# Kernel tuning notes

Hardware: AMD Instinct MI355X
Metric: run time of the kernel (lower is better)

## Reference

```python
import jax, jax.numpy as jnp
import numpy as np

EPS = 1e-12  # tf.math.l2_normalize epsilon


def get_posenc(n, d):
    # Standard sinusoidal positional encoding, shape [n, d].
    pos = np.arange(n)[:, None].astype(np.float32)
    i = np.arange(d)[None, :]
    angle_rates = 1.0 / np.power(10000.0, (2 * (i // 2)).astype(np.float32) / np.float32(d))
    angles = pos * angle_rates
    pe = np.zeros((n, d), dtype=np.float32)
    pe[:, 0::2] = np.sin(angles[:, 0::2])
    pe[:, 1::2] = np.cos(angles[:, 1::2])
    return jnp.asarray(pe)


def setup_inputs() -> dict:
    key = jax.random.key(0)
    k1, k2, k3 = jax.random.split(key, 3)
    B, N, D = 4, 2048, 2048  # N must equal D (model_size) for the posenc matmul
    data = jax.random.normal(k1, (B, N, D), dtype=jnp.float32)
    W_exp = jax.random.normal(k2, (D + 1, D), dtype=jnp.float32) * (1.0 / np.sqrt(D + 1))
    b_exp = jnp.zeros((D,), dtype=jnp.float32)
    W_merge = jax.random.normal(k3, (2 * D, D), dtype=jnp.float32) * (1.0 / np.sqrt(2 * D))
    return {"data": data, "W_exp": W_exp, "b_exp": b_exp, "W_merge": W_merge}


def reference(data, W_exp, b_exp, W_merge):
    B, N, D = data.shape
    # l2 normalize along feature dim
    sq = jnp.sum(data * data, axis=-1, keepdims=True)
    cn = data * jax.lax.rsqrt(jnp.maximum(sq, EPS))
    # pairwise cosine similarity, rectified: [B, N, N]
    sim = jax.nn.relu(jnp.einsum("bnd,bmd->bnm", cn, cn))
    # fixed positional matmul: posenc [N, D] with D == N -> [B, N, N]
    fixed_v = get_posenc(N, D)
    v_output = jnp.einsum("nk,bkm->bnm", fixed_v, sim)
    # row-sum of similarities: [B, N, 1]
    csum = jnp.sum(sim, axis=-1, keepdims=True)
    counter = jnp.concatenate([csum, v_output], axis=-1)  # [B, N, N+1]
    counter = jax.nn.softplus(counter @ W_exp + b_exp)  # [B, N, D]
    out = jnp.concatenate([data, counter], axis=-1) @ W_merge  # [B, N, D]
    return out
```

## Files before the change

### kernel.cpp

```cpp
#include <hip/hip_runtime.h>

#define B_ 4
#define N_ 2048
#define D_ 2048

#define BM 128
#define BN 128
#define BK 32
#define TP 136

typedef __bf16 bf16x8 __attribute__((ext_vector_type(8)));
typedef float  f32x4  __attribute__((ext_vector_type(4)));

__device__ __forceinline__ ushort f2bf(float x) {
  union { float f; unsigned u; } c; c.f = x;
  unsigned u = c.u;
  u += 0x7fffu + ((u >> 16) & 1u);
  return (ushort)(u >> 16);
}

__device__ __forceinline__ void gld16(ushort* lds, const ushort* g) {
  __builtin_amdgcn_global_load_lds(
      (const __attribute__((address_space(1))) void*)g,
      (__attribute__((address_space(3))) void*)lds, 16, 0, 0);
}


__global__ void prep_cn(const float* __restrict__ data, ushort* __restrict__ cn,
                        ushort* __restrict__ catA) {
  const int row = blockIdx.x;
  const long base = (long)row * D_;
  const float4* r4 = (const float4*)(data + base);
  const int tid = threadIdx.x;
  float4 u0 = r4[tid * 2], u1 = r4[tid * 2 + 1];
  float s = u0.x*u0.x + u0.y*u0.y + u0.z*u0.z + u0.w*u0.w
          + u1.x*u1.x + u1.y*u1.y + u1.z*u1.z + u1.w*u1.w;
  #pragma unroll
  for (int o = 32; o > 0; o >>= 1) s += __shfl_down(s, o);
  __shared__ float wsum[4];
  if ((tid & 63) == 0) wsum[tid >> 6] = s;
  __syncthreads();
  const float tot = wsum[0] + wsum[1] + wsum[2] + wsum[3];
  const float sc = rsqrtf(fmaxf(tot, 1e-12f));
  uint4 pc, pd;
  pc.x = (unsigned)f2bf(u0.x * sc) | ((unsigned)f2bf(u0.y * sc) << 16);
  pc.y = (unsigned)f2bf(u0.z * sc) | ((unsigned)f2bf(u0.w * sc) << 16);
  pc.z = (unsigned)f2bf(u1.x * sc) | ((unsigned)f2bf(u1.y * sc) << 16);
  pc.w = (unsigned)f2bf(u1.z * sc) | ((unsigned)f2bf(u1.w * sc) << 16);
  pd.x = (unsigned)f2bf(u0.x) | ((unsigned)f2bf(u0.y) << 16);
  pd.y = (unsigned)f2bf(u0.z) | ((unsigned)f2bf(u0.w) << 16);
  pd.z = (unsigned)f2bf(u1.x) | ((unsigned)f2bf(u1.y) << 16);
  pd.w = (unsigned)f2bf(u1.z) | ((unsigned)f2bf(u1.w) << 16);
  *(uint4*)(cn + base + tid * 8) = pc;
  *(uint4*)(catA + (long)row * (2 * D_) + tid * 8) = pd;
}

__global__ void prep_pe(ushort* __restrict__ pe) {
  const int id = blockIdx.x * 256 + threadIdx.x;
  const int n = id >> 11, d = id & (D_ - 1);
  const float e = (float)(2 * (d >> 1)) * (1.0f / (float)D_);
  const float rate = expf(e * -9.210340371976184f);
  const float ang = (float)n * rate;
  const float v = (d & 1) ? cosf(ang) : sinf(ang);
  pe[id] = f2bf(v);
}

__global__ void transpose_bf16(const float* __restrict__ in, ushort* __restrict__ out,
                               int R, int C) {
  __shared__ float t[32][33];
  const int c0 = blockIdx.x * 32, r0 = blockIdx.y * 32;
  const int tx = threadIdx.x, ty = threadIdx.y;
  #pragma unroll
  for (int i = 0; i < 32; i += 8) t[ty + i][tx] = in[(long)(r0 + ty + i) * C + c0 + tx];
  __syncthreads();
  #pragma unroll
  for (int i = 0; i < 32; i += 8) out[(long)(c0 + ty + i) * R + r0 + tx] = f2bf(t[tx][ty + i]);
}

__global__ __launch_bounds__(256, 2) void gemm_sym(
    const ushort* __restrict__ Ag, ushort* __restrict__ Cg, float* __restrict__ csum) {
  __shared__ ushort sAt[BM * BK];
  __shared__ ushort sBt[BN * BK];
  __shared__ ushort tile[128 * TP];

  const int bz = blockIdx.z;
  const int t = blockIdx.x;
  int bj = (int)((sqrtf(8.f * (float)t + 1.f) - 1.f) * 0.5f);
  while ((bj + 1) * (bj + 2) / 2 <= t) bj++;
  while (bj * (bj + 1) / 2 > t) bj--;
  const int bi = t - bj * (bj + 1) / 2;

  const ushort* A = Ag + (long)bz * N_ * D_;
  const int blockRow = bi * BM;
  const int blockCol = bj * BN;

  const int tid = threadIdx.x;
  const int w = tid >> 6, L = tid & 63;
  const int ldRow = w * 16 + (L >> 2);
  const int ldK = (((L & 3) ^ ((L >> 3) & 3)) * 8);
  const ushort* a0 = A + (long)(blockRow + ldRow) * D_ + ldK;
  const ushort* a1 = a0 + (long)64 * D_;
  const ushort* b0 = A + (long)(blockCol + ldRow) * D_ + ldK;
  const ushort* b1 = b0 + (long)64 * D_;
  ushort* sA0 = sAt + w * 512;
  ushort* sA1 = sAt + 2048 + w * 512;
  ushort* sB0 = sBt + w * 512;
  ushort* sB1 = sBt + 2048 + w * 512;

  const int wm = (w & 1) * 64, wn = (w >> 1) * 64;
  const int fr = L & 15;
  const int sw = (((L >> 4) ^ ((fr >> 1) & 3)) * 8);

  f32x4 acc[4][4] = {};
  for (int k0 = 0; k0 < D_; k0 += BK) {
    gld16(sA0, a0); gld16(sA1, a1);
    gld16(sB0, b0); gld16(sB1, b1);
    a0 += BK; a1 += BK; b0 += BK; b1 += BK;
    __syncthreads();
    bf16x8 af[4], bfv[4];
    #pragma unroll
    for (int i = 0; i < 4; i++) af[i]  = *(const bf16x8*)&sAt[(wm + i * 16 + fr) * BK + sw];
    #pragma unroll
    for (int j = 0; j < 4; j++) bfv[j] = *(const bf16x8*)&sBt[(wn + j * 16 + fr) * BK + sw];
    #pragma unroll
    for (int i = 0; i < 4; i++)
      #pragma unroll
      for (int j = 0; j < 4; j++)
        acc[i][j] = __builtin_amdgcn_mfma_f32_16x16x32_bf16(af[i], bfv[j], acc[i][j], 0, 0, 0);
    __syncthreads();
  }

  const int rq = (L >> 4) * 4;
  const int cq = L & 15;
  ushort* C = Cg + (long)bz * N_ * N_;

  float rs[4][4];
  float cs[4];
  #pragma unroll
  for (int i = 0; i < 4; i++)
    #pragma unroll
    for (int r = 0; r < 4; r++) rs[i][r] = 0.f;
  #pragma unroll
  for (int j = 0; j < 4; j++) cs[j] = 0.f;

  const bool offdiag = (bi != bj);
  #pragma unroll
  for (int i = 0; i < 4; i++)
    #pragma unroll
    for (int j = 0; j < 4; j++)
      #pragma unroll
      for (int r = 0; r < 4; r++) {
        const float v = fmaxf(acc[i][j][r], 0.f);
        const int lrow = wm + i * 16 + rq + r;
        const int lcol = wn + j * 16 + cq;
        const ushort bv = f2bf(v);
        C[(long)(blockRow + lrow) * N_ + blockCol + lcol] = bv;
        rs[i][r] += v;
        cs[j] += v;
        if (offdiag) tile[lcol * TP + lrow] = bv;
      }

  #pragma unroll
  for (int i = 0; i < 4; i++)
    #pragma unroll
    for (int r = 0; r < 4; r++) {
      float s = rs[i][r];
      s += __shfl_xor(s, 1); s += __shfl_xor(s, 2);
      s += __shfl_xor(s, 4); s += __shfl_xor(s, 8);
      if (cq == 0)
        atomicAdd(&csum[(long)bz * N_ + blockRow + wm + i * 16 + rq + r], s);
    }

  if (offdiag) {
    #pragma unroll
    for (int j = 0; j < 4; j++) {
      float s = cs[j];
      s += __shfl_xor(s, 16); s += __shfl_xor(s, 32);
      if (L < 16)
        atomicAdd(&csum[(long)bz * N_ + blockCol + wn + j * 16 + cq], s);
    }
    __syncthreads();
    const int rp = tid >> 1, h = tid & 1;
    const ushort* src = &tile[rp * TP + h * 64];
    ushort* dst = &C[(long)(blockCol + rp) * N_ + blockRow + h * 64];
    #pragma unroll
    for (int q = 0; q < 8; q++)
      *(uint4*)(dst + q * 8) = *(const uint4*)(src + q * 8);
  }
}

template <int MODE>
__global__ __launch_bounds__(256, 2) void gemm_bt(
    const ushort* __restrict__ Ag, const ushort* __restrict__ Bg, void* __restrict__ Cg,
    int K, long sA, long sB, long sC, int ldc, int colOff,
    const float* __restrict__ csum, const float* __restrict__ w0,
    const float* __restrict__ bexp) {
  __shared__ ushort sAt[BM * BK];
  __shared__ ushort sBt[BN * BK];

  const int lin = blockIdx.x + (blockIdx.y << 4) + (blockIdx.z << 8);
  const int xcd = lin & 7, m = lin >> 3;
  const int bz = xcd >> 1;
  const int by = ((xcd & 1) << 3) + (m >> 4);
  const int bx = m & 15;

  const ushort* A  = Ag + (long)bz * sA;
  const ushort* Bp = Bg + (long)bz * sB;

  const int tid = threadIdx.x;
  const int w = tid >> 6, L = tid & 63;
  const int blockRow = bx * BM;
  const int blockCol = by * BN;

  const int ldRow = w * 16 + (L >> 2);
  const int ldK = (((L & 3) ^ ((L >> 3) & 3)) * 8);
  const ushort* a0 = A  + (long)(blockRow + ldRow) * K + ldK;
  const ushort* a1 = a0 + (long)64 * K;
  const ushort* b0 = Bp + (long)(blockCol + ldRow) * K + ldK;
  const ushort* b1 = b0 + (long)64 * K;
  ushort* sA0 = sAt + w * 512;
  ushort* sA1 = sAt + 2048 + w * 512;
  ushort* sB0 = sBt + w * 512;
  ushort* sB1 = sBt + 2048 + w * 512;

  const int wm = (w & 1) * 64, wn = (w >> 1) * 64;
  const int fr = L & 15;
  const int sw = (((L >> 4) ^ ((fr >> 1) & 3)) * 8);

  f32x4 acc[4][4] = {};
  for (int k0 = 0; k0 < K; k0 += BK) {
    gld16(sA0, a0); gld16(sA1, a1);
    gld16(sB0, b0); gld16(sB1, b1);
    a0 += BK; a1 += BK; b0 += BK; b1 += BK;
    __syncthreads();
    bf16x8 af[4], bfv[4];
    #pragma unroll
    for (int i = 0; i < 4; i++) af[i]  = *(const bf16x8*)&sAt[(wm + i * 16 + fr) * BK + sw];
    #pragma unroll
    for (int j = 0; j < 4; j++) bfv[j] = *(const bf16x8*)&sBt[(wn + j * 16 + fr) * BK + sw];
    #pragma unroll
    for (int i = 0; i < 4; i++)
      #pragma unroll
      for (int j = 0; j < 4; j++)
        acc[i][j] = __builtin_amdgcn_mfma_f32_16x16x32_bf16(af[i], bfv[j], acc[i][j], 0, 0, 0);
    __syncthreads();
  }

  const int rq = (L >> 4) * 4;
  const int cq = L & 15;

  if (MODE == 1) {
    ushort* C = (ushort*)Cg + (long)bz * sC;
    #pragma unroll
    for (int i = 0; i < 4; i++)
      #pragma unroll
      for (int j = 0; j < 4; j++)
        #pragma unroll
        for (int r = 0; r < 4; r++) {
          const int row = blockRow + wm + i * 16 + rq + r;
          const int col = blockCol + wn + j * 16 + cq;
          C[(long)row * ldc + col] = f2bf(acc[i][j][r]);
        }
  } else if (MODE == 2) {
    ushort* C = (ushort*)Cg + (long)bz * sC;
    #pragma unroll
    for (int i = 0; i < 4; i++)
      #pragma unroll
      for (int j = 0; j < 4; j++)
        #pragma unroll
        for (int r = 0; r < 4; r++) {
          const int row = blockRow + wm + i * 16 + rq + r;
          const int col = blockCol + wn + j * 16 + cq;
          const float x = acc[i][j][r] + csum[(long)bz * N_ + row] * w0[col] + bexp[col];
          const float sp = fmaxf(x, 0.f) + log1pf(expf(-fabsf(x)));
          C[(long)row * ldc + colOff + col] = f2bf(sp);
        }
  } else {
    float* C = (float*)Cg + (long)bz * sC;
    #pragma unroll
    for (int i = 0; i < 4; i++)
      #pragma unroll
      for (int j = 0; j < 4; j++)
        #pragma unroll
        for (int r = 0; r < 4; r++) {
          const int row = blockRow + wm + i * 16 + rq + r;
          const int col = blockCol + wn + j * 16 + cq;
          C[(long)row * ldc + col] = acc[i][j][r];
        }
  }
}

extern "C" void kernel_launch(void* const* d_in, const int* in_sizes, int n_in,
                              void* d_out, int out_size, void* d_ws, size_t ws_size,
                              hipStream_t stream) {
  const float* data    = (const float*)d_in[0];
  const float* W_exp   = (const float*)d_in[1];
  const float* b_exp   = (const float*)d_in[2];
  const float* W_merge = (const float*)d_in[3];

  char* ws = (char*)d_ws;
  const size_t MB = 1024 * 1024;
  ushort* cnv  = (ushort*)(ws);
  ushort* sim  = (ushort*)(ws + 32 * MB);
  ushort* pe   = (ushort*)(ws + 64 * MB);
  ushort* weT  = (ushort*)(ws + 72 * MB);
  ushort* wmT  = (ushort*)(ws + 80 * MB);
  ushort* catA = (ushort*)(ws + 96 * MB);
  float*  csum = (float*)(ws + 160 * MB);

  hipMemsetAsync(csum, 0, (size_t)B_ * N_ * sizeof(float), stream);
  prep_cn<<<B_ * N_, 256, 0, stream>>>(data, cnv, catA);
  prep_pe<<<(N_ * N_) / 256, 256, 0, stream>>>(pe);
  transpose_bf16<<<dim3(D_ / 32, D_ / 32), dim3(32, 8), 0, stream>>>(W_exp + D_, weT, D_, D_);
  transpose_bf16<<<dim3(D_ / 32, (2 * D_) / 32), dim3(32, 8), 0, stream>>>(W_merge, wmT, 2 * D_, D_);

  dim3 blk(256);
  gemm_sym<<<dim3(136, 1, B_), blk, 0, stream>>>(cnv, sim, csum);
  dim3 g(N_ / BM, N_ / BN, B_);
  gemm_bt<1><<<g, blk, 0, stream>>>(pe, sim, cnv, N_, 0, (long)N_ * N_,
                                    (long)N_ * N_, N_, 0, nullptr, nullptr, nullptr);
  gemm_bt<2><<<g, blk, 0, stream>>>(cnv, weT, catA, N_, (long)N_ * N_, 0,
                                    (long)N_ * 2 * D_, 2 * D_, D_, csum, W_exp, b_exp);
  gemm_bt<3><<<g, blk, 0, stream>>>(catA, wmT, d_out, 2 * D_, (long)N_ * 2 * D_, 0,
                                    (long)N_ * D_, D_, 0, nullptr, nullptr, nullptr);
}
```

Baseline: 561.9 us.

## Replace 128x128 GEMMs with 256x256 eight-wave double-buffered pipelined kernel

Replaces the three dense bf16 GEMMs with a 256x256-tile, 512-thread kernel. It uses 128KB of dynamic LDS with double-buffered BK=64 stages, and interleaves global-to-LDS prefetch with MFMA phases under explicit barriers, vmcnt waits and setprio. The aim is more data reuse per tile and hiding of load latency behind compute, where the old kernel waited on each K step with two syncthreads. In exchange, the larger tiles mean fewer blocks (256 per GEMM) and occupancy is limited by LDS. The hand-scheduled waitcnt logic is fragile.

```diff
diff --git a/kernel.cpp b/kernel.cpp
--- a/kernel.cpp
+++ b/kernel.cpp
@@ -189,103 +189,153 @@
   }
 }
 
+
+__device__ __forceinline__ void stage_half(ushort* d, const ushort* s, int K) {
+  gld16(d, s);
+  gld16(d + 4096, s + (long)64 * K);
+}
+
+template <int M0, bool FIRST, class STG>
+__device__ __forceinline__ void phase8(const ushort* __restrict__ TA,
+                                       const ushort* __restrict__ TB,
+                                       int aO0, int aO1, int bO0, int bO1,
+                                       bf16x8 (&bf)[4][2], f32x4 (&acc)[8][4],
+                                       int vm, STG&& stg) {
+  if (FIRST) {
+    #pragma unroll
+    for (int j = 0; j < 4; j++) {
+      bf[j][0] = *(const bf16x8*)&TB[bO0 + j * 1024];
+      bf[j][1] = *(const bf16x8*)&TB[bO1 + j * 1024];
+    }
+  }
+  bf16x8 af[2][2];
+  #pragma unroll
+  for (int mm = 0; mm < 2; mm++) {
+    af[mm][0] = *(const bf16x8*)&TA[aO0 + (M0 + mm) * 1024];
+    af[mm][1] = *(const bf16x8*)&TA[aO1 + (M0 + mm) * 1024];
+  }
+  __builtin_amdgcn_sched_barrier(0);
+  stg();
+  asm volatile("s_barrier" ::: "memory");
+  asm volatile("s_waitcnt lgkmcnt(0)" ::: "memory");
+  __builtin_amdgcn_sched_barrier(0);
+  __builtin_amdgcn_s_setprio(1);
+  #pragma unroll
+  for (int kk = 0; kk < 2; kk++)
+    #pragma unroll
+    for (int mm = 0; mm < 2; mm++)
+      #pragma unroll
+      for (int j = 0; j < 4; j++)
+        acc[M0 + mm][j] = __builtin_amdgcn_mfma_f32_16x16x32_bf16(
+            af[mm][kk], bf[j][kk], acc[M0 + mm][j], 0, 0, 0);
+  __builtin_amdgcn_s_setprio(0);
+  if (vm == 6)      asm volatile("s_waitcnt vmcnt(6)" ::: "memory");
+  else if (vm == 0) asm volatile("s_waitcnt vmcnt(0)" ::: "memory");
+  asm volatile("s_barrier" ::: "memory");
+}
+
 template <int MODE>
-__global__ __launch_bounds__(256, 2) void gemm_bt(
+__global__ __launch_bounds__(512, 2) void gemm8(
     const ushort* __restrict__ Ag, const ushort* __restrict__ Bg, void* __restrict__ Cg,
     int K, long sA, long sB, long sC, int ldc, int colOff,
     const float* __restrict__ csum, const float* __restrict__ w0,
     const float* __restrict__ bexp) {
-  __shared__ ushort sAt[BM * BK];
-  __shared__ ushort sBt[BN * BK];
-
-  const int lin = blockIdx.x + (blockIdx.y << 4) + (blockIdx.z << 8);
-  const int xcd = lin & 7, m = lin >> 3;
+  extern __shared__ ushort lds[];
+
+  const int lin = blockIdx.x + (blockIdx.y << 3) + (blockIdx.z << 6);
+  const int xcd = lin & 7, m_ = lin >> 3;
   const int bz = xcd >> 1;
-  const int by = ((xcd & 1) << 3) + (m >> 4);
-  const int bx = m & 15;
-
-  const ushort* A  = Ag + (long)bz * sA;
-  const ushort* Bp = Bg + (long)bz * sB;
+  const int by = ((xcd & 1) << 2) + (m_ >> 3);
+  const int bx = m_ & 7;
+
+  const ushort* A  = Ag + (long)bz * sA + (long)(bx << 8) * K;
+  const ushort* Bp = Bg + (long)bz * sB + (long)(by << 8) * K;
 
   const int tid = threadIdx.x;
-  const int w = tid >> 6, L = tid & 63;
-  const int blockRow = bx * BM;
-  const int blockCol = by * BN;
-
-  const int ldRow = w * 16 + (L >> 2);
-  const int ldK = (((L & 3) ^ ((L >> 3) & 3)) * 8);
-  const ushort* a0 = A  + (long)(blockRow + ldRow) * K + ldK;
-  const ushort* a1 = a0 + (long)64 * K;
-  const ushort* b0 = Bp + (long)(blockCol + ldRow) * K + ldK;
-  const ushort* b1 = b0 + (long)64 * K;
-  ushort* sA0 = sAt + w * 512;
-  ushort* sA1 = sAt + 2048 + w * 512;
-  ushort* sB0 = sBt + w * 512;
-  ushort* sB1 = sBt + 2048 + w * 512;
-
-  const int wm = (w & 1) * 64, wn = (w >> 1) * 64;
-  const int fr = L & 15;
-  const int sw = (((L >> 4) ^ ((fr >> 1) & 3)) * 8);
-
-  f32x4 acc[4][4] = {};
-  for (int k0 = 0; k0 < K; k0 += BK) {
-    gld16(sA0, a0); gld16(sA1, a1);
-    gld16(sB0, b0); gld16(sB1, b1);
-    a0 += BK; a1 += BK; b0 += BK; b1 += BK;
-    __syncthreads();
-    bf16x8 af[4], bfv[4];
-    #pragma unroll
-    for (int i = 0; i < 4; i++) af[i]  = *(const bf16x8*)&sAt[(wm + i * 16 + fr) * BK + sw];
-    #pragma unroll
-    for (int j = 0; j < 4; j++) bfv[j] = *(const bf16x8*)&sBt[(wn + j * 16 + fr) * BK + sw];
-    #pragma unroll
-    for (int i = 0; i < 4; i++)
-      #pragma unroll
-      for (int j = 0; j < 4; j++)
-        acc[i][j] = __builtin_amdgcn_mfma_f32_16x16x32_bf16(af[i], bfv[j], acc[i][j], 0, 0, 0);
-    __syncthreads();
-  }
-
-  const int rq = (L >> 4) * 4;
-  const int cq = L & 15;
-
-  if (MODE == 1) {
-    ushort* C = (ushort*)Cg + (long)bz * sC;
-    #pragma unroll
-    for (int i = 0; i < 4; i++)
+  const int sr = tid >> 3;
+  const int sc = ((tid & 7) ^ (sr & 7)) << 3;
+  const ushort* aS = A + (long)sr * K + sc;
+  const ushort* bS = Bp + (long)sr * K + sc;
+  const int wOff = (tid >> 6) << 9;
+  ushort* const stA0 = lds + wOff;
+  ushort* const stA1 = lds + 16384 + wOff;
+  ushort* const stB0 = lds + 32768 + wOff;
+  ushort* const stB1 = lds + 49152 + wOff;
+  const ushort* const TA0 = lds;          const ushort* const TA1 = lds + 16384;
+  const ushort* const TB0 = lds + 32768;  const ushort* const TB1 = lds + 49152;
+
+  auto stg = [&](ushort* base, const ushort* src, int T, int H) {
+    stage_half(base + (H << 13), src + (long)(H << 7) * K + ((long)T << 6), K);
+  };
+
+  const int L = tid & 63, wid = tid >> 6;
+  const int wr = wid >> 2, wc = wid & 3;
+  const int fr = L & 15, g = L >> 4;
+  const int off0 = ((g ^ (fr & 7)) << 3);
+  const int aO0 = ((wr << 7) + fr) * 64 + off0, aO1 = aO0 ^ 32;
+  const int bO0 = ((wc << 6) + fr) * 64 + off0, bO1 = bO0 ^ 32;
+
+  f32x4 acc[8][4] = {};
+  bf16x8 bf[4][2];
+
+  const int NT = K >> 6, NTI = NT >> 1;
+
+  stg(stB0, bS, 0, 0); stg(stB0, bS, 0, 1); stg(stA0, aS, 0, 0); stg(stA0, aS, 0, 1);
+  stg(stB1, bS, 1, 0); stg(stB1, bS, 1, 1); stg(stA1, aS, 1, 0); stg(stA1, aS, 1, 1);
+  asm volatile("s_waitcnt vmcnt(6)" ::: "memory");
+  asm volatile("s_barrier" ::: "memory");
+
+  for (int it = 0; it < NTI; ++it) {
+    const int T2 = 2 * it + 2;
+    const bool more = (it + 1 < NTI);
+    phase8<0, true >(TA0, TB0, aO0, aO1, bO0, bO1, bf, acc, -1, [&] {});
+    phase8<2, false>(TA0, TB0, aO0, aO1, bO0, bO1, bf, acc, -1,
+                     [&] { if (more) stg(stB0, bS, T2, 0); });
+    phase8<4, false>(TA0, TB0, aO0, aO1, bO0, bO1, bf, acc, -1,
+                     [&] { if (more) stg(stB0, bS, T2, 1); });
+    phase8<6, false>(TA0, TB0, aO0, aO1, bO0, bO1, bf, acc, more ? 6 : 0,
+                     [&] { if (more) { stg(stA0, aS, T2, 0); stg(stA0, aS, T2, 1); } });
+    phase8<0, true >(TA1, TB1, aO0, aO1, bO0, bO1, bf, acc, -1, [&] {});
+    phase8<2, false>(TA1, TB1, aO0, aO1, bO0, bO1, bf, acc, -1,
+                     [&] { if (more) stg(stB1, bS, T2 + 1, 0); });
+    phase8<4, false>(TA1, TB1, aO0, aO1, bO0, bO1, bf, acc, -1,
+                     [&] { if (more) stg(stB1, bS, T2 + 1, 1); });
+    phase8<6, false>(TA1, TB1, aO0, aO1, bO0, bO1, bf, acc, more ? 6 : -1,
+                     [&] { if (more) { stg(stA1, aS, T2 + 1, 0); stg(stA1, aS, T2 + 1, 1); } });
+  }
+
+  const int rq = g << 2, cq = fr;
+  const int rowB0 = (bx << 8) + (wr << 7);
+  const int colB0 = (by << 8) + (wc << 6);
+  if (MODE == 3) {
+    float* C = (float*)Cg + (long)bz * sC;
+    #pragma unroll
+    for (int m = 0; m < 8; m++)
       #pragma unroll
       for (int j = 0; j < 4; j++)
         #pragma unroll
         for (int r = 0; r < 4; r++) {
-          const int row = blockRow + wm + i * 16 + rq + r;
-          const int col = blockCol + wn + j * 16 + cq;
-          C[(long)row * ldc + col] = f2bf(acc[i][j][r]);
+          const int row = rowB0 + m * 16 + rq + r;
+          const int col = colB0 + j * 16 + cq;
+          C[(long)row * ldc + col] = acc[m][j][r];
         }
-  } else if (MODE == 2) {
+  } else {
     ushort* C = (ushort*)Cg + (long)bz * sC;
     #pragma unroll
-    for (int i = 0; i < 4; i++)
+    for (int m = 0; m < 8; m++)
       #pragma unroll
       for (int j = 0; j < 4; j++)
         #pragma unroll
         for (int r = 0; r < 4; r++) {
-          const int row = blockRow + wm + i * 16 + rq + r;
-          const int col = blockCol + wn + j * 16 + cq;
-          const float x = acc[i][j][r] + csum[(long)bz * N_ + row] * w0[col] + bexp[col];
-          const float sp = fmaxf(x, 0.f) + log1pf(expf(-fabsf(x)));
-          C[(long)row * ldc + colOff + col] = f2bf(sp);
-        }
-  } else {
-    float* C = (float*)Cg + (long)bz * sC;
-    #pragma unroll
-    for (int i = 0; i < 4; i++)
-      #pragma unroll
-      for (int j = 0; j < 4; j++)
-        #pragma unroll
-        for (int r = 0; r < 4; r++) {
-          const int row = blockRow + wm + i * 16 + rq + r;
-          const int col = blockCol + wn + j * 16 + cq;
-          C[(long)row * ldc + col] = acc[i][j][r];
+          const int row = rowB0 + m * 16 + rq + r;
+          const int col = colB0 + j * 16 + cq;
+          if (MODE == 1) {
+            C[(long)row * ldc + col] = f2bf(acc[m][j][r]);
+          } else {
+            const float x = acc[m][j][r] + csum[(long)bz * N_ + row] * w0[col] + bexp[col];
+            const float sp = fmaxf(x, 0.f) + log1pf(expf(-fabsf(x)));
+            C[(long)row * ldc + colOff + col] = f2bf(sp);
+          }
         }
   }
 }
@@ -308,19 +358,27 @@
   ushort* catA = (ushort*)(ws + 96 * MB);
   float*  csum = (float*)(ws + 160 * MB);
 
+  static bool attrs_set = false;
+  if (!attrs_set) {
+    hipFuncSetAttribute((const void*)gemm8<1>, hipFuncAttributeMaxDynamicSharedMemorySize, 131072);
+    hipFuncSetAttribute((const void*)gemm8<2>, hipFuncAttributeMaxDynamicSharedMemorySize, 131072);
+    hipFuncSetAttribute((const void*)gemm8<3>, hipFuncAttributeMaxDynamicSharedMemorySize, 131072);
+    attrs_set = true;
+  }
+
   hipMemsetAsync(csum, 0, (size_t)B_ * N_ * sizeof(float), stream);
   prep_cn<<<B_ * N_, 256, 0, stream>>>(data, cnv, catA);
   prep_pe<<<(N_ * N_) / 256, 256, 0, stream>>>(pe);
   transpose_bf16<<<dim3(D_ / 32, D_ / 32), dim3(32, 8), 0, stream>>>(W_exp + D_, weT, D_, D_);
   transpose_bf16<<<dim3(D_ / 32, (2 * D_) / 32), dim3(32, 8), 0, stream>>>(W_merge, wmT, 2 * D_, D_);
 
-  dim3 blk(256);
-  gemm_sym<<<dim3(136, 1, B_), blk, 0, stream>>>(cnv, sim, csum);
-  dim3 g(N_ / BM, N_ / BN, B_);
-  gemm_bt<1><<<g, blk, 0, stream>>>(pe, sim, cnv, N_, 0, (long)N_ * N_,
-                                    (long)N_ * N_, N_, 0, nullptr, nullptr, nullptr);
-  gemm_bt<2><<<g, blk, 0, stream>>>(cnv, weT, catA, N_, (long)N_ * N_, 0,
-                                    (long)N_ * 2 * D_, 2 * D_, D_, csum, W_exp, b_exp);
-  gemm_bt<3><<<g, blk, 0, stream>>>(catA, wmT, d_out, 2 * D_, (long)N_ * 2 * D_, 0,
-                                    (long)N_ * D_, D_, 0, nullptr, nullptr, nullptr);
-}
+  gemm_sym<<<dim3(136, 1, B_), dim3(256), 0, stream>>>(cnv, sim, csum);
+
+  dim3 g8(N_ / 256, N_ / 256, B_);
+  gemm8<1><<<g8, 512, 131072, stream>>>(pe, sim, cnv, N_, 0, (long)N_ * N_,
+                                        (long)N_ * N_, N_, 0, nullptr, nullptr, nullptr);
+  gemm8<2><<<g8, 512, 131072, stream>>>(cnv, weT, catA, N_, (long)N_ * N_, 0,
+                                        (long)N_ * 2 * D_, 2 * D_, D_, csum, W_exp, b_exp);
+  gemm8<3><<<g8, 512, 131072, stream>>>(catA, wmT, d_out, 2 * D_, (long)N_ * 2 * D_, 0,
+                                        (long)N_ * D_, D_, 0, nullptr, nullptr, nullptr);
+}
```

Measured after the change: 529.6 us. -5.7%, faster.
